# Performance work log

Measured on AMD Instinct MI355X. Metric: run time of the kernel, lower is better.

Reference implementation:

```python
import jax, jax.numpy as jnp
import numpy as np

N, E, DN, DE, H, L = 2048, 32768, 512, 512, 8, 2
BN_EPS = 1e-5  # torch BatchNorm1d eps; eval mode with running_mean=0, running_var=1


def setup_inputs():
    key = jax.random.key(0)
    ks = jax.random.split(key, 12)
    rng = np.random.default_rng(0)
    # unique directed edges: 3E/4 upper-triangular pairs + reverses of the first E/4
    iu, ju = np.triu_indices(N, k=1)
    sel = rng.choice(iu.size, size=3 * E // 4, replace=False)
    s, d = iu[sel], ju[sel]
    src = np.concatenate([s, d[: E // 4]])
    dst = np.concatenate([d, s[: E // 4]])
    edge_index = jnp.asarray(np.stack([src, dst]).astype(np.int32))

    def p(k, shape, fan_in):
        return jax.random.normal(k, shape, jnp.float32) / np.sqrt(fan_in).astype(np.float32)

    return dict(
        x=jax.random.normal(ks[0], (N, DN), jnp.float32),
        edge_feature=jax.random.normal(ks[1], (E, DE), jnp.float32),
        node_pos=jax.random.uniform(ks[2], (N, 3), jnp.float32) * 10.0,
        inw=p(ks[3], (L, 3 * DN, DN), DN),          # MHA in_proj_weight per layer
        inb=jnp.zeros((L, 3 * DN), jnp.float32),
        ow=p(ks[4], (L, DN, DN), DN),               # MHA out_proj
        ob=jnp.zeros((L, DN), jnp.float32),
        etw=p(ks[5], (L, DE, DE), DE),              # edge_transform Linear
        etb=jnp.zeros((L, DE), jnp.float32),
        etg=jnp.ones((L, DE), jnp.float32),         # edge_transform BN gamma
        etbb=jnp.zeros((L, DE), jnp.float32),       # edge_transform BN beta
        unw=p(ks[6], (L, DN, DN + DE), DN + DE),    # update_node Linear
        unb=jnp.zeros((L, DN), jnp.float32),
        uew=p(ks[7], (L, DE, 2 * DN + 2 * DE), 2 * DN + 2 * DE),  # update_edge Linear
        ueb=jnp.zeros((L, DE), jnp.float32),
        edge_index=edge_index,
    )


def _forward(x, edge_feature, node_pos, inw, inb, ow, ob, etw, etb, etg, etbb, unw, unb, uew, ueb, edge_index):
    src, dst = edge_index[0], edge_index[1]
    n, e = x.shape[0], src.shape[0]
    hd = DN // H
    # vectorized reverse-edge lookup (mirrors the torch edge_dict)
    keys = src * n + dst
    rkeys = dst * n + src
    order = jnp.argsort(keys)
    sk = keys[order]
    pos = jnp.clip(jnp.searchsorted(sk, rkeys), 0, e - 1)
    found = sk[pos] == rkeys
    rev_idx = order[pos]
    # distance-based attention mask: -inf everywhere, 1/(dist+eps) on (symmetric) edges, 1.0 on diagonal
    diff = node_pos[src] - node_pos[dst]
    w = 1.0 / (jnp.sqrt(jnp.sum(diff * diff, axis=-1)) + 1e-6)
    mask = jnp.full((n, n), -jnp.inf, x.dtype)
    mask = mask.at[src, dst].set(w).at[dst, src].set(w)
    diag = jnp.arange(n)
    mask = mask.at[diag, diag].set(1.0)
    bn_scale = np.float32(1.0 / np.sqrt(1.0 + BN_EPS))
    nf, ef = x, edge_feature
    for l in range(L):
        rev = jnp.where(found[:, None], ef[rev_idx], 0.0)
        # MHSA over all nodes as one sequence (batch=1), eval mode (dropout off)
        qkv = nf @ inw[l].T + inb[l]
        q, k, v = [t.reshape(n, H, hd) for t in jnp.split(qkv, 3, axis=-1)]
        scores = jnp.einsum('nhd,mhd->hnm', q * np.float32(1.0 / np.sqrt(hd)), k) + mask
        attn = jax.nn.softmax(scores, axis=-1)
        ctx = jnp.einsum('hnm,mhd->nhd', attn, v).reshape(n, DN)
        x_upd = ctx @ ow[l].T + ob[l]
        # message: update_edge on [x_i, e, e_rev, x_j] (flow=target_to_source -> x_i = x[src])
        upd_edge = jnp.concatenate([nf[src], ef, rev, nf[dst]], axis=1) @ uew[l].T + ueb[l]
        # edge_transform = Linear + BN(eval) + ReLU
        te = jax.nn.relu((ef @ etw[l].T + etb[l]) * bn_scale * etg[l] + etbb[l])
        # scatter-max to subject/object nodes (empty segments -> 0, torch_scatter convention)
        subj = jax.ops.segment_max(te, src, num_segments=n)
        obj = jax.ops.segment_max(te, dst, num_segments=n)
        subj = jnp.where(jnp.isneginf(subj), 0.0, subj)
        obj = jnp.where(jnp.isneginf(obj), 0.0, obj)
        nf = jnp.concatenate([x_upd, subj + obj], axis=1) @ unw[l].T + unb[l]
        ef = upd_edge
        if l < L - 1 or L == 1:
            nf = jax.nn.relu(nf)
            ef = jax.nn.relu(ef)
    return nf, ef


def reference(x, edge_feature, node_pos, inw, inb, ow, ob, etw, etb, etg, etbb, unw, unb, uew, ueb, edge_index):
    return _forward(x, edge_feature, node_pos, inw, inb, ow, ob, etw, etb, etg, etbb, unw, unb, uew, ueb, edge_index)
```

## Files before the change

kernel.cpp:

```cpp
#include <hip/hip_runtime.h>
#include <hip/hip_bf16.h>

#define NN 2048
#define EE 32768
#define DND 512
#define NH 8
#define HD 64
#define MAXD 128
#define NEGF (-1e30f)
#define BN_SCALE 0.9999950000374997f

typedef __attribute__((ext_vector_type(8))) short bf16x8;
typedef __attribute__((ext_vector_type(4))) float f32x4;
typedef unsigned short u16;
typedef unsigned int u32;

static __device__ __forceinline__ float4 ld4(const float* p) {
    return *reinterpret_cast<const float4*>(p);
}
static __device__ __forceinline__ u16 f2b(float f) {
    __hip_bfloat16 h = __float2bfloat16(f);
    return *reinterpret_cast<u16*>(&h);
}
static __device__ __forceinline__ float b2f(u32 bits) {
    return __uint_as_float(bits << 16);
}
static __device__ __forceinline__ void gl_lds(const u16* g, u16* l) {
    __builtin_amdgcn_global_load_lds((const __attribute__((address_space(1))) void*)g,
                                     (__attribute__((address_space(3))) void*)l, 16, 0, 0);
}


__global__ __launch_bounds__(256) void init_table_k(int* __restrict__ t) {
    int i = blockIdx.x * 256 + threadIdx.x;
    t[i] = -1;
}

__global__ __launch_bounds__(256) void fill_table_k(const int* __restrict__ ei, int* __restrict__ t) {
    int e = blockIdx.x * 256 + threadIdx.x;
    if (e < EE) t[(size_t)ei[e] * NN + ei[EE + e]] = e;
}

__global__ __launch_bounds__(256) void build_rev_k(const int* __restrict__ ei, const int* __restrict__ t,
                                                   int* __restrict__ rev) {
    int e = blockIdx.x * 256 + threadIdx.x;
    if (e < EE) rev[e] = t[(size_t)ei[EE + e] * NN + ei[e]];
}

__global__ __launch_bounds__(256) void init_csr_k(int* __restrict__ adj, float* __restrict__ wadj,
                                                  int* __restrict__ cnt) {
    int i = blockIdx.x * 256 + threadIdx.x;
    if (i < NN) { cnt[i] = 1; adj[i * MAXD] = i; wadj[i * MAXD] = 1.0f; }
}

__global__ __launch_bounds__(256) void fill_csr_k(const int* __restrict__ ei, const int* __restrict__ rev,
                                                  const float* __restrict__ pos,
                                                  int* __restrict__ adj, float* __restrict__ wadj,
                                                  int* __restrict__ cnt) {
    int e = blockIdx.x * 256 + threadIdx.x;
    if (e >= EE) return;
    int s = ei[e], d = ei[EE + e];
    float dx = pos[s * 3 + 0] - pos[d * 3 + 0];
    float dy = pos[s * 3 + 1] - pos[d * 3 + 1];
    float dz = pos[s * 3 + 2] - pos[d * 3 + 2];
    float w = 1.0f / (sqrtf(dx * dx + dy * dy + dz * dz) + 1e-6f);
    int slot = atomicAdd(&cnt[s], 1);
    if (slot < MAXD) { adj[s * MAXD + slot] = d; wadj[s * MAXD + slot] = w; }
    if (rev[e] < 0) {
        slot = atomicAdd(&cnt[d], 1);
        if (slot < MAXD) { adj[d * MAXD + slot] = s; wadj[d * MAXD + slot] = w; }
    }
}

__global__ __launch_bounds__(256) void init_ecsr_k(int* __restrict__ ocnt, int* __restrict__ icnt) {
    int i = blockIdx.x * 256 + threadIdx.x;
    if (i < NN) { ocnt[i] = 0; icnt[i] = 0; }
}

__global__ __launch_bounds__(256) void fill_ecsr_k(const int* __restrict__ ei,
                                                   int* __restrict__ oadj, int* __restrict__ ocnt,
                                                   int* __restrict__ iadj, int* __restrict__ icnt) {
    int e = blockIdx.x * 256 + threadIdx.x;
    if (e >= EE) return;
    int s = ei[e], d = ei[EE + e];
    int slot = atomicAdd(&ocnt[s], 1);
    if (slot < MAXD) oadj[s * MAXD + slot] = e;
    slot = atomicAdd(&icnt[d], 1);
    if (slot < MAXD) iadj[d * MAXD + slot] = e;
}

__global__ __launch_bounds__(256) void conv_k(const float* __restrict__ src, u16* __restrict__ dst) {
    int i = (blockIdx.x * 256 + threadIdx.x) * 8;
    float4 a = ld4(src + i), b = ld4(src + i + 4);
    u16 o[8];
    o[0] = f2b(a.x); o[1] = f2b(a.y); o[2] = f2b(a.z); o[3] = f2b(a.w);
    o[4] = f2b(b.x); o[5] = f2b(b.y); o[6] = f2b(b.z); o[7] = f2b(b.w);
    *reinterpret_cast<int4*>(dst + i) = *reinterpret_cast<const int4*>(o);
}

__global__ __launch_bounds__(256) void gather_max_k(const u16* __restrict__ te,
                                                    const int* __restrict__ oadj, const int* __restrict__ ocnt,
                                                    const int* __restrict__ iadj, const int* __restrict__ icnt,
                                                    u16* __restrict__ sums)
{
    const int i = blockIdx.x;
    const int c2 = threadIdx.x;
    float ms0 = 0.f, ms1 = 0.f, mo0 = 0.f, mo1 = 0.f;
    int no = ocnt[i]; if (no > MAXD) no = MAXD;
    for (int s = 0; s < no; ++s) {
        const int e = oadj[i * MAXD + s];
        const u32 v = *reinterpret_cast<const u32*>(te + (size_t)e * DND + c2 * 2);
        ms0 = fmaxf(ms0, b2f(v & 0xffffu));
        ms1 = fmaxf(ms1, b2f(v >> 16));
    }
    int ni = icnt[i]; if (ni > MAXD) ni = MAXD;
    for (int s = 0; s < ni; ++s) {
        const int e = iadj[i * MAXD + s];
        const u32 v = *reinterpret_cast<const u32*>(te + (size_t)e * DND + c2 * 2);
        mo0 = fmaxf(mo0, b2f(v & 0xffffu));
        mo1 = fmaxf(mo1, b2f(v >> 16));
    }
    const u32 r = (u32)f2b(ms0 + mo0) | ((u32)f2b(ms1 + mo1) << 16);
    *reinterpret_cast<u32*>(sums + (size_t)i * DND + c2 * 2) = r;
}

template <int MODE, int EPI, int WF32, int WBF16, int GY>
__global__ __launch_bounds__(256) void mgemm_k(
    const u16* __restrict__ WS, u32 a_off, u32 b_off, const float* __restrict__ bias,
    float* __restrict__ Cf, u16* __restrict__ Cb, int M, int Nc, int K,
    u32 g0_off, u32 g1_off, u32 gz_off,
    const int* __restrict__ srcv, const int* __restrict__ dstv, const int* __restrict__ revv,
    const float* __restrict__ eg, const float* __restrict__ eb)
{
    __shared__ u16 As2[2][8192];
    __shared__ u16 Bs2[2][8192];
    const int tid = threadIdx.x, lane = tid & 63, w = tid >> 6;
    const int wr = w >> 1, wc = w & 1;
    const int b = blockIdx.x;
    const int xcd = b & 7, kb = b >> 3;
    const int bm = ((kb / GY) * 8 + xcd) * 128;
    const int bn = (kb % GY) * 128;

    const int rl = lane >> 3;
    const u32 lx = (u32)(((lane & 7) ^ rl) * 8);

    u32 offA0[4], offA1[4], offB[4];
#pragma unroll
    for (int q = 0; q < 4; ++q) {
        const int ra = bm + w * 32 + q * 8 + rl;
        if (MODE == 0) {
            offA0[q] = a_off + (u32)ra * (u32)K + lx;
        } else {
            offA0[q] = g0_off + (u32)ra * 512u + lx;
            offA1[q] = g1_off + (u32)ra * 512u + lx;
        }
        offB[q] = b_off + (u32)(bn + w * 32 + q * 8 + rl) * (u32)K + lx;
    }

    const int nks = K >> 6;
    const int kq = lane >> 4, li = lane & 15;

    auto stage = [&](int t, int buf) {
        const u32 k0 = (u32)t * 64u;
        const int seg = (MODE == 0) ? 0 : (int)(k0 >> 9);
#pragma unroll
        for (int q = 0; q < 4; ++q) {
            u32 oa = (MODE == 0) ? offA0[q] : (seg == 0 ? offA0[q] : offA1[q]);
            const u32 koff = (MODE == 0) ? k0 : (k0 & 511u);
            gl_lds(WS + oa + koff, &As2[buf][(w * 32 + q * 8) * 64]);
        }
#pragma unroll
        for (int q = 0; q < 4; ++q)
            gl_lds(WS + offB[q] + k0, &Bs2[buf][(w * 32 + q * 8) * 64]);
    };

    f32x4 acc[4][4] = {};
    const int baseA = (wr * 64 + li) * 64 + ((kq ^ (li & 7)) * 8);
    const int baseB = (wc * 64 + li) * 64 + ((kq ^ (li & 7)) * 8);

    stage(0, 0);
    for (int t = 0; t < nks; ++t) {
        const int cur = t & 1;
        if (t + 1 < nks) stage(t + 1, cur ^ 1);
        if (t + 1 < nks) asm volatile("s_waitcnt vmcnt(8)" ::: "memory");
        else             asm volatile("s_waitcnt vmcnt(0)" ::: "memory");
        __builtin_amdgcn_s_barrier();
        __builtin_amdgcn_sched_barrier(0);
#pragma unroll
        for (int sub = 0; sub < 2; ++sub) {
            const int sx = sub << 5;
            bf16x8 af[4], bf[4];
#pragma unroll
            for (int m = 0; m < 4; ++m)
                af[m] = *reinterpret_cast<const bf16x8*>(&As2[cur][(baseA + m * 1024) ^ sx]);
#pragma unroll
            for (int n = 0; n < 4; ++n)
                bf[n] = *reinterpret_cast<const bf16x8*>(&Bs2[cur][(baseB + n * 1024) ^ sx]);
#pragma unroll
            for (int m = 0; m < 4; ++m)
#pragma unroll
                for (int n = 0; n < 4; ++n)
                    acc[m][n] = __builtin_amdgcn_mfma_f32_16x16x32_bf16(af[m], bf[n], acc[m][n], 0, 0, 0);
        }
        __builtin_amdgcn_s_barrier();
        __builtin_amdgcn_sched_barrier(0);
    }

    float bsv[4], scv[4], shv[4];
#pragma unroll
    for (int n = 0; n < 4; ++n) {
        const int col = bn + wc * 64 + n * 16 + li;
        bsv[n] = bias[col];
        if (EPI == 2) { scv[n] = BN_SCALE * eg[col]; shv[n] = eb[col]; }
    }
#pragma unroll
    for (int m = 0; m < 4; ++m) {
#pragma unroll
        for (int n = 0; n < 4; ++n) {
            const int col = bn + wc * 64 + n * 16 + li;
#pragma unroll
            for (int i = 0; i < 4; ++i) {
                float v = acc[m][n][i] + bsv[n];
                if (EPI == 2) v = fmaxf(fmaf(v, scv[n], shv[n]), 0.f);
                else if (EPI == 1) v = fmaxf(v, 0.f);
                const int r = bm + wr * 64 + m * 16 + (lane >> 4) * 4 + i;
                if (WF32) Cf[(size_t)r * Nc + col] = v;
                if (WBF16) Cb[(size_t)r * Nc + col] = f2b(v);
            }
        }
    }
}

template <int MODE, int EPI, int WF32, int WBF16>
__global__ __launch_bounds__(512, 2) void mgemm256_k(
    const u16* __restrict__ WS, u32 a_off, u32 b_off, const float* __restrict__ bias,
    float* __restrict__ Cf, u16* __restrict__ Cb, int M, int Nc, int K,
    u32 g0_off, u32 g1_off, u32 gz_off,
    const int* __restrict__ srcv, const int* __restrict__ dstv, const int* __restrict__ revv,
    const float* __restrict__ eg, const float* __restrict__ eb)
{
    __shared__ u16 SB[65536];
    const int tid = threadIdx.x, lane = tid & 63, w = tid >> 6;
    const int wr = w >> 2, wc = w & 3;
    const int b = blockIdx.x;
    const int bm = ((b & 7) + 8 * (b >> 4)) * 256;
    const int bn = ((b >> 3) & 1) * 256;

    const int rl = lane >> 3;
    const u32 lx = (u32)(((lane & 7) ^ rl) * 8);

    u32 offA0[4], offA1[4], offA2[4], offA3[4], offB[4];
#pragma unroll
    for (int q = 0; q < 4; ++q) {
        const int ra = bm + w * 32 + q * 8 + rl;
        if (MODE == 0) {
            offA0[q] = a_off + (u32)ra * (u32)K + lx;
        } else {
            offA0[q] = g0_off + (u32)srcv[ra] * 512u + lx;
            offA1[q] = g1_off + (u32)ra * 512u + lx;
            const int rv = revv[ra];
            offA2[q] = (rv >= 0 ? g1_off + (u32)rv * 512u : gz_off) + lx;
            offA3[q] = g0_off + (u32)dstv[ra] * 512u + lx;
        }
        offB[q] = b_off + (u32)(bn + w * 32 + q * 8 + rl) * (u32)K + lx;
    }

    const int nks = K >> 6;
    const int kq = lane >> 4, li = lane & 15;

    auto stage = [&](int t, int buf) {
        const u32 k0 = (u32)t * 64u;
        const int seg = (MODE == 0) ? 0 : (int)(k0 >> 9);
#pragma unroll
        for (int q = 0; q < 4; ++q) {
            u32 oa;
            if (MODE == 0) oa = offA0[q];
            else           oa = (seg == 0 ? offA0[q] : seg == 1 ? offA1[q] : seg == 2 ? offA2[q] : offA3[q]);
            const u32 koff = (MODE == 0) ? k0 : (k0 & 511u);
            gl_lds(WS + oa + koff, &SB[buf * 16384 + (w * 32 + q * 8) * 64]);
        }
#pragma unroll
        for (int q = 0; q < 4; ++q)
            gl_lds(WS + offB[q] + k0, &SB[32768 + buf * 16384 + (w * 32 + q * 8) * 64]);
    };

    f32x4 acc[8][4] = {};
    const int baseA = (wr * 128 + li) * 64 + ((kq ^ (li & 7)) * 8);
    const int baseB = (wc * 64 + li) * 64 + ((kq ^ (li & 7)) * 8);

    stage(0, 0);
    for (int t = 0; t < nks; ++t) {
        const int cur = t & 1;
        if (t + 1 < nks) stage(t + 1, cur ^ 1);
        if (t + 1 < nks) asm volatile("s_waitcnt vmcnt(8)" ::: "memory");
        else             asm volatile("s_waitcnt vmcnt(0)" ::: "memory");
        __builtin_amdgcn_s_barrier();
        __builtin_amdgcn_sched_barrier(0);
#pragma unroll
        for (int sub = 0; sub < 2; ++sub) {
            const int sx = sub << 5;
            bf16x8 af[8], bf[4];
#pragma unroll
            for (int m = 0; m < 8; ++m)
                af[m] = *reinterpret_cast<const bf16x8*>(&SB[(cur * 16384 + baseA + m * 1024) ^ sx]);
#pragma unroll
            for (int n = 0; n < 4; ++n)
                bf[n] = *reinterpret_cast<const bf16x8*>(&SB[(32768 + cur * 16384 + baseB + n * 1024) ^ sx]);
#pragma unroll
            for (int m = 0; m < 8; ++m)
#pragma unroll
                for (int n = 0; n < 4; ++n)
                    acc[m][n] = __builtin_amdgcn_mfma_f32_16x16x32_bf16(af[m], bf[n], acc[m][n], 0, 0, 0);
        }
        __builtin_amdgcn_s_barrier();
        __builtin_amdgcn_sched_barrier(0);
    }

    float bsv[4], scv[4], shv[4];
#pragma unroll
    for (int n = 0; n < 4; ++n) {
        const int col = bn + wc * 64 + n * 16 + li;
        bsv[n] = bias[col];
        if (EPI == 2) { scv[n] = BN_SCALE * eg[col]; shv[n] = eb[col]; }
    }
#pragma unroll
    for (int m = 0; m < 8; ++m) {
#pragma unroll
        for (int n = 0; n < 4; ++n) {
            const int col = bn + wc * 64 + n * 16 + li;
#pragma unroll
            for (int i = 0; i < 4; ++i) {
                float v = acc[m][n][i] + bsv[n];
                if (EPI == 2) v = fmaxf(fmaf(v, scv[n], shv[n]), 0.f);
                else if (EPI == 1) v = fmaxf(v, 0.f);
                const int r = bm + wr * 128 + m * 16 + (lane >> 4) * 4 + i;
                if (WF32) Cf[(size_t)r * Nc + col] = v;
                if (WBF16) Cb[(size_t)r * Nc + col] = f2b(v);
            }
        }
    }
}

__global__ __launch_bounds__(256) void attn_sp_k(const float* __restrict__ qkv,
                                                 const int* __restrict__ adj,
                                                 const float* __restrict__ wadj,
                                                 const int* __restrict__ cnt,
                                                 u16* __restrict__ ctxb)
{
    const int i = blockIdx.x;
    const int wv = threadIdx.x >> 6, lane = threadIdx.x & 63;
    const int h = blockIdx.y * 4 + wv;
    __shared__ float qs[4][64];
    qs[wv][lane] = qkv[(size_t)i * 1536 + h * HD + lane] * 0.125f;
    __syncthreads();
    int deg = cnt[i];
    if (deg > MAXD) deg = MAXD;
    float m = -3.0e38f, lsum = 0.f, c = 0.f;
    for (int base = 0; base < deg; base += 64) {
        int nn_ = deg - base; if (nn_ > 64) nn_ = 64;
        int j = 0;
        float s = NEGF;
        if (lane < nn_) {
            j = adj[i * MAXD + base + lane];
            const float wgt = wadj[i * MAXD + base + lane];
            const float* kr = qkv + (size_t)j * 1536 + DND + h * HD;
            float accd = 0.f;
#pragma unroll
            for (int d4 = 0; d4 < 16; ++d4) {
                float4 kv = ld4(kr + d4 * 4);
                accd = fmaf(qs[wv][d4 * 4 + 0], kv.x, accd);
                accd = fmaf(qs[wv][d4 * 4 + 1], kv.y, accd);
                accd = fmaf(qs[wv][d4 * 4 + 2], kv.z, accd);
                accd = fmaf(qs[wv][d4 * 4 + 3], kv.w, accd);
            }
            s = accd + wgt;
        }
        float mloc = s;
#pragma unroll
        for (int o = 1; o < 64; o <<= 1) mloc = fmaxf(mloc, __shfl_xor(mloc, o, 64));
        const float mnew = fmaxf(m, mloc);
        const float alpha = __expf(m - mnew);
        const float p = (lane < nn_) ? __expf(s - mnew) : 0.f;
        float ps = p;
#pragma unroll
        for (int o = 1; o < 64; o <<= 1) ps += __shfl_xor(ps, o, 64);
        lsum = lsum * alpha + ps;
        c *= alpha;
        for (int l = 0; l < nn_; ++l) {
            const float pj = __shfl(p, l, 64);
            const int jj = __shfl(j, l, 64);
            c = fmaf(pj, qkv[(size_t)jj * 1536 + 2 * DND + h * HD + lane], c);
        }
        m = mnew;
    }
    ctxb[(size_t)i * DND + h * HD + lane] = f2b(c / lsum);
}

extern "C" void kernel_launch(void* const* d_in, const int* in_sizes, int n_in,
                              void* d_out, int out_size, void* d_ws, size_t ws_size,
                              hipStream_t stream)
{
    const float* x    = (const float*)d_in[0];
    const float* efin = (const float*)d_in[1];
    const float* pos  = (const float*)d_in[2];
    const float* inw  = (const float*)d_in[3];
    const float* inb  = (const float*)d_in[4];
    const float* ow   = (const float*)d_in[5];
    const float* ob   = (const float*)d_in[6];
    const float* etw  = (const float*)d_in[7];
    const float* etb  = (const float*)d_in[8];
    const float* etg  = (const float*)d_in[9];
    const float* etbb = (const float*)d_in[10];
    const float* unw  = (const float*)d_in[11];
    const float* unb  = (const float*)d_in[12];
    const float* uew  = (const float*)d_in[13];
    const float* ueb  = (const float*)d_in[14];
    const int*   ei   = (const int*)d_in[15];

    float* W = (float*)d_ws;
    float* qkv   = W;
    u16*   te    = (u16*)W;
    int*   rev   = (int*)(W + 8388608);
    u16*   zero  = (u16*)(W + 8421376);
    int*   adj   = (int*)(W + 8421888);
    float* wadj  = W + 8684032;
    int*   cnt   = (int*)(W + 8946176);
    int*   oadj  = (int*)(W + 8948224);
    int*   ocnt  = (int*)(W + 9210368);
    int*   iadj  = (int*)(W + 9212416);
    int*   icnt  = (int*)(W + 9474560);
    u16*   ctxb  = (u16*)(W + 9476608);
    u16*   xupdb = (u16*)(W + 10000896);
    u16*   sums  = (u16*)(W + 10525184);
    u16*   nfb   = (u16*)(W + 11049472);
    u16*   wbf   = (u16*)(W + 11573760);
    u16*   efbA  = (u16*)(W + 14457344);
    u16*   efbB  = (u16*)(W + 22845952);
    int*   table = (int*)efbA;

    u16* inwb = wbf;
    u16* owb  = wbf + 1572864;
    u16* etwb = wbf + 2097152;
    u16* unwb = wbf + 2621440;
    u16* uewb = wbf + 3670016;

    float* out_nf = (float*)d_out;
    float* out_ef = out_nf + (size_t)NN * DND;

    const int* srcv = ei;
    const int* dstv = ei + EE;

    const u16* WSu = (const u16*)d_ws;
    auto uoff = [&](const void* p) { return (u32)((const u16*)p - WSu); };

    init_table_k<<<NN * NN / 256, 256, 0, stream>>>(table);
    fill_table_k<<<EE / 256, 256, 0, stream>>>(ei, table);
    build_rev_k<<<EE / 256, 256, 0, stream>>>(ei, table, rev);
    init_csr_k<<<NN / 256, 256, 0, stream>>>(adj, wadj, cnt);
    fill_csr_k<<<EE / 256, 256, 0, stream>>>(ei, rev, pos, adj, wadj, cnt);
    init_ecsr_k<<<NN / 256, 256, 0, stream>>>(ocnt, icnt);
    fill_ecsr_k<<<EE / 256, 256, 0, stream>>>(ei, oadj, ocnt, iadj, icnt);
    hipMemsetAsync(zero, 0, 2048, stream);

    conv_k<<<1572864 / 2048, 256, 0, stream>>>(inw, inwb);
    conv_k<<<524288 / 2048, 256, 0, stream>>>(ow, owb);
    conv_k<<<524288 / 2048, 256, 0, stream>>>(etw, etwb);
    conv_k<<<1048576 / 2048, 256, 0, stream>>>(unw, unwb);
    conv_k<<<2097152 / 2048, 256, 0, stream>>>(uew, uewb);
    conv_k<<<1048576 / 2048, 256, 0, stream>>>(x, nfb);
    conv_k<<<16777216 / 2048, 256, 0, stream>>>(efin, efbA);

    for (int l = 0; l < 2; ++l) {
        const u16* efb_cur = l ? efbB : efbA;
        const u16* inwb_l = inwb + (size_t)l * 786432;
        const u16* owb_l  = owb  + (size_t)l * 262144;
        const u16* etwb_l = etwb + (size_t)l * 262144;
        const u16* unwb_l = unwb + (size_t)l * 524288;
        const u16* uewb_l = uewb + (size_t)l * 1048576;
        const float* inb_l  = inb  + (size_t)l * 1536;
        const float* ob_l   = ob   + (size_t)l * 512;
        const float* etb_l  = etb  + (size_t)l * 512;
        const float* etg_l  = etg  + (size_t)l * 512;
        const float* etbb_l = etbb + (size_t)l * 512;
        const float* unb_l  = unb  + (size_t)l * 512;
        const float* ueb_l  = ueb  + (size_t)l * 512;

        mgemm_k<0, 0, 1, 0, 12><<<192, 256, 0, stream>>>(
            WSu, uoff(nfb), uoff(inwb_l), inb_l, qkv, nullptr, NN, 1536, DND,
            0, 0, 0, nullptr, nullptr, nullptr, nullptr, nullptr);

        attn_sp_k<<<dim3(NN, 2), 256, 0, stream>>>(qkv, adj, wadj, cnt, ctxb);

        mgemm_k<0, 0, 0, 1, 4><<<64, 256, 0, stream>>>(
            WSu, uoff(ctxb), uoff(owb_l), ob_l, nullptr, xupdb, NN, DND, DND,
            0, 0, 0, nullptr, nullptr, nullptr, nullptr, nullptr);

        mgemm256_k<0, 2, 0, 1><<<256, 512, 0, stream>>>(
            WSu, uoff(efb_cur), uoff(etwb_l), etb_l, nullptr, te, EE, DND, DND,
            0, 0, 0, nullptr, nullptr, nullptr, etg_l, etbb_l);

        gather_max_k<<<NN, 256, 0, stream>>>(te, oadj, ocnt, iadj, icnt, sums);

        if (l == 0)
            mgemm256_k<1, 1, 0, 1><<<256, 512, 0, stream>>>(
                WSu, 0, uoff(uewb_l), ueb_l, nullptr, efbB, EE, DND, 2048,
                uoff(nfb), uoff(efb_cur), uoff(zero), srcv, dstv, rev, nullptr, nullptr);
        else
            mgemm256_k<1, 0, 1, 0><<<256, 512, 0, stream>>>(
                WSu, 0, uoff(uewb_l), ueb_l, out_ef, nullptr, EE, DND, 2048,
                uoff(nfb), uoff(efb_cur), uoff(zero), srcv, dstv, rev, nullptr, nullptr);

        if (l == 0)
            mgemm_k<2, 1, 0, 1, 4><<<64, 256, 0, stream>>>(
                WSu, 0, uoff(unwb_l), unb_l, nullptr, nfb, NN, DND, 1024,
                uoff(xupdb), uoff(sums), 0, nullptr, nullptr, nullptr, nullptr, nullptr);
        else
            mgemm_k<2, 0, 1, 0, 4><<<64, 256, 0, stream>>>(
                WSu, 0, uoff(unwb_l), unb_l, out_nf, nullptr, NN, DND, 1024,
                uoff(xupdb), uoff(sums), 0, nullptr, nullptr, nullptr, nullptr, nullptr);
    }
}
```

Measured before the change: 468.5 us.

## Interleave next-tile global-to-LDS prefetch with MFMA chunks in GEMM main loop

Splits the next k-tile's global-to-LDS loads into four pairs and issues them spread across the MFMA sub-blocks instead of all at the loop top. The A fragment loads are split into two halves, and each MFMA burst is wrapped in s_setprio raises so compute and memory issue interleave. This aims to hide load issue latency and cut register pressure from the af array. It risks scheduler constraints from the added sched_barriers and a changed vmcnt accounting.

```diff
diff --git a/kernel.cpp b/kernel.cpp
--- a/kernel.cpp
+++ b/kernel.cpp
@@ -268,19 +268,22 @@
     const int nks = K >> 6;
     const int kq = lane >> 4, li = lane & 15;
 
-    auto stage = [&](int t, int buf) {
+    auto stageA2 = [&](int t, int buf, int q0) {
         const u32 k0 = (u32)t * 64u;
         const int seg = (MODE == 0) ? 0 : (int)(k0 >> 9);
-#pragma unroll
-        for (int q = 0; q < 4; ++q) {
+        const u32 koff = (MODE == 0) ? k0 : (k0 & 511u);
+#pragma unroll
+        for (int q = q0; q < q0 + 2; ++q) {
             u32 oa;
             if (MODE == 0) oa = offA0[q];
             else           oa = (seg == 0 ? offA0[q] : seg == 1 ? offA1[q] : seg == 2 ? offA2[q] : offA3[q]);
-            const u32 koff = (MODE == 0) ? k0 : (k0 & 511u);
             gl_lds(WS + oa + koff, &SB[buf * 16384 + (w * 32 + q * 8) * 64]);
         }
-#pragma unroll
-        for (int q = 0; q < 4; ++q)
+    };
+    auto stageB2 = [&](int t, int buf, int q0) {
+        const u32 k0 = (u32)t * 64u;
+#pragma unroll
+        for (int q = q0; q < q0 + 2; ++q)
             gl_lds(WS + offB[q] + k0, &SB[32768 + buf * 16384 + (w * 32 + q * 8) * 64]);
     };
 
@@ -288,29 +291,47 @@
     const int baseA = (wr * 128 + li) * 64 + ((kq ^ (li & 7)) * 8);
     const int baseB = (wc * 64 + li) * 64 + ((kq ^ (li & 7)) * 8);
 
-    stage(0, 0);
+    stageA2(0, 0, 0); stageA2(0, 0, 2); stageB2(0, 0, 0); stageB2(0, 0, 2);
     for (int t = 0; t < nks; ++t) {
         const int cur = t & 1;
-        if (t + 1 < nks) stage(t + 1, cur ^ 1);
-        if (t + 1 < nks) asm volatile("s_waitcnt vmcnt(8)" ::: "memory");
-        else             asm volatile("s_waitcnt vmcnt(0)" ::: "memory");
+        const bool pf = (t + 1 < nks);
+        if (pf) {
+            stageA2(t + 1, cur ^ 1, 0);
+            asm volatile("s_waitcnt vmcnt(2)" ::: "memory");
+        } else {
+            asm volatile("s_waitcnt vmcnt(0)" ::: "memory");
+        }
         __builtin_amdgcn_s_barrier();
         __builtin_amdgcn_sched_barrier(0);
 #pragma unroll
         for (int sub = 0; sub < 2; ++sub) {
             const int sx = sub << 5;
-            bf16x8 af[8], bf[4];
-#pragma unroll
-            for (int m = 0; m < 8; ++m)
-                af[m] = *reinterpret_cast<const bf16x8*>(&SB[(cur * 16384 + baseA + m * 1024) ^ sx]);
+            bf16x8 bf[4];
 #pragma unroll
             for (int n = 0; n < 4; ++n)
                 bf[n] = *reinterpret_cast<const bf16x8*>(&SB[(32768 + cur * 16384 + baseB + n * 1024) ^ sx]);
 #pragma unroll
-            for (int m = 0; m < 8; ++m)
-#pragma unroll
-                for (int n = 0; n < 4; ++n)
-                    acc[m][n] = __builtin_amdgcn_mfma_f32_16x16x32_bf16(af[m], bf[n], acc[m][n], 0, 0, 0);
+            for (int mh = 0; mh < 2; ++mh) {
+                if (pf) {
+                    if (sub == 0 && mh == 0)      stageA2(t + 1, cur ^ 1, 2);
+                    else if (sub == 0 && mh == 1) stageB2(t + 1, cur ^ 1, 0);
+                    else if (sub == 1 && mh == 0) stageB2(t + 1, cur ^ 1, 2);
+                }
+                bf16x8 af[4];
+#pragma unroll
+                for (int m = 0; m < 4; ++m)
+                    af[m] = *reinterpret_cast<const bf16x8*>(&SB[(cur * 16384 + baseA + (mh * 4 + m) * 1024) ^ sx]);
+                __builtin_amdgcn_sched_barrier(0);
+                __builtin_amdgcn_s_setprio(1);
+#pragma unroll
+                for (int m = 0; m < 4; ++m)
+#pragma unroll
+                    for (int n = 0; n < 4; ++n)
+                        acc[mh * 4 + m][n] =
+                            __builtin_amdgcn_mfma_f32_16x16x32_bf16(af[m], bf[n], acc[mh * 4 + m][n], 0, 0, 0);
+                __builtin_amdgcn_s_setprio(0);
+                __builtin_amdgcn_sched_barrier(0);
+            }
         }
         __builtin_amdgcn_s_barrier();
         __builtin_amdgcn_sched_barrier(0);
```

Result: no change. 463.8 us (-1.0%).
